# Kernel tuning notes

Measured on AMD Instinct MI355X. Metric: run time of the kernel, lower is better.

## Reference

```python
import jax, jax.numpy as jnp
import numpy as np

D, DFF, H = 768, 3072, 12
HD = D // H
EPS = 1e-12

def _ln(t, gamma, beta):
    mu = t.mean(-1, keepdims=True)
    var = jnp.mean((t - mu) ** 2, -1, keepdims=True)
    return gamma * (t - mu) / jnp.sqrt(var + EPS) + beta

def setup_inputs() -> dict:
    key = jax.random.key(0)
    ks = jax.random.split(key, 16)
    s = 0.02
    x = jax.random.normal(ks[0], (2, 2048, D), jnp.float32)
    mask = jnp.ones((2, 2048), jnp.float32)
    def lin(k, out_d, in_d):
        kw, kb = jax.random.split(k)
        return (jax.random.normal(kw, (out_d, in_d), jnp.float32) * s,
                jnp.zeros((out_d,), jnp.float32))
    Wq, bq = lin(ks[1], D, D)
    Wk, bk = lin(ks[2], D, D)
    Wv, bv = lin(ks[3], D, D)
    Wp, bp = lin(ks[4], D, D)
    W1, bf1 = lin(ks[5], DFF, D)
    W2, bf2 = lin(ks[6], D, DFF)
    g1 = jnp.ones((D,), jnp.float32); be1 = jnp.zeros((D,), jnp.float32)
    g2 = jnp.ones((D,), jnp.float32); be2 = jnp.zeros((D,), jnp.float32)
    return dict(x=x, mask=mask, Wq=Wq, bq=bq, Wk=Wk, bk=bk, Wv=Wv, bv=bv,
                Wp=Wp, bp=bp, g1=g1, be1=be1, W1=W1, bf1=bf1, W2=W2, bf2=bf2,
                g2=g2, be2=be2)

def reference(x, mask, Wq, bq, Wk, bk, Wv, bv, Wp, bp, g1, be1, W1, bf1, W2, bf2, g2, be2):
    B, S, _ = x.shape
    # projections (torch Linear: x @ W^T + b)
    q = (x @ Wq.T + bq).reshape(B, S, H, HD).transpose(0, 2, 1, 3)  # [B,H,S,HD]
    k = (x @ Wk.T + bk).reshape(B, S, H, HD).transpose(0, 2, 1, 3)
    v = (x @ Wv.T + bv).reshape(B, S, H, HD).transpose(0, 2, 1, 3)
    scores = jnp.einsum('bhqd,bhkd->bhqk', q, k) / jnp.sqrt(jnp.float32(HD))
    scores = scores - 10000.0 * (1.0 - mask[:, None, None, :])
    p = jax.nn.softmax(scores, axis=-1)  # dropout is identity at eval
    h = jnp.einsum('bhqk,bhkd->bqhd', p, v).reshape(B, S, D)
    h = h @ Wp.T + bp
    x1 = _ln(x + h, g1, be1)
    ff = jax.nn.gelu(x1 @ W1.T + bf1, approximate=False) @ W2.T + bf2
    return _ln(x1 + ff, g2, be2)
```

## Files before the change

### kernel.cpp

```cpp
#include <hip/hip_runtime.h>
#include <hip/hip_bf16.h>
#include <math.h>

#define D_MODEL 768
#define D_FF    3072
#define N_HEAD  12
#define HEAD_D  64
#define BATCH   2
#define SEQ     2048
#define QKV_LD  2304

typedef __attribute__((ext_vector_type(8))) short short8;
typedef __attribute__((ext_vector_type(8))) unsigned short ushort8;
typedef __attribute__((ext_vector_type(4))) float f32x4;

__device__ inline unsigned short f2bf(float f) {
    union { __hip_bfloat16 b; unsigned short u; } cv;
    cv.b = __float2bfloat16(f);
    return cv.u;
}

__device__ inline float bf2f(unsigned short u) {
    union { unsigned int i; float f; } cv;
    cv.i = ((unsigned int)u) << 16;
    return cv.f;
}

__device__ inline void async_load16(const void* g, void* l) {
    __builtin_amdgcn_global_load_lds(
        (const __attribute__((address_space(1))) void*)g,
        (__attribute__((address_space(3))) void*)l, 16, 0, 0);
}

__global__ __launch_bounds__(256) void conv_fused(
    const float* __restrict__ x,
    const float* __restrict__ Wq, const float* __restrict__ Wk,
    const float* __restrict__ Wv, const float* __restrict__ Wp,
    const float* __restrict__ W1, const float* __restrict__ W2,
    const float* __restrict__ bq, const float* __restrict__ bk,
    const float* __restrict__ bv,
    unsigned short* __restrict__ xb, unsigned short* __restrict__ wqkvb,
    unsigned short* __restrict__ wpb, unsigned short* __restrict__ w1b,
    unsigned short* __restrict__ w2b, float* __restrict__ bqkv)
{
    int bid = blockIdx.x;
    const float* src; unsigned short* dst; int base;
    if      (bid < 3072) { src = x;  dst = xb;              base = bid;        }
    else if (bid < 3648) { src = Wq; dst = wqkvb;           base = bid - 3072; }
    else if (bid < 4224) { src = Wk; dst = wqkvb + 589824;  base = bid - 3648; }
    else if (bid < 4800) { src = Wv; dst = wqkvb + 1179648; base = bid - 4224; }
    else if (bid < 5376) { src = Wp; dst = wpb;             base = bid - 4800; }
    else if (bid < 7680) { src = W1; dst = w1b;             base = bid - 5376; }
    else if (bid < 9984) { src = W2; dst = w2b;             base = bid - 7680; }
    else {
        for (int j = threadIdx.x; j < QKV_LD; j += 256)
            bqkv[j] = (j < 768) ? bq[j] : (j < 1536) ? bk[j - 768] : bv[j - 1536];
        return;
    }
    int i = (base * 256 + threadIdx.x) * 4;
    float4 v = *(const float4*)(src + i);
    ushort4 o4;
    o4.x = f2bf(v.x); o4.y = f2bf(v.y); o4.z = f2bf(v.z); o4.w = f2bf(v.w);
    *(ushort4*)(dst + i) = o4;
}

#define NSTAGE 3

__global__ __launch_bounds__(256) void gemm_bf16(
    const unsigned short* __restrict__ A, int lda,
    const unsigned short* __restrict__ W, int ldw,
    const float* __restrict__ bias,
    const unsigned short* __restrict__ resb, int ldr,
    float* __restrict__ outf, unsigned short* __restrict__ outb,
    float* __restrict__ pacc, int ldo,
    int M, int N, int K, int mode)
{
    __shared__ unsigned short As[NSTAGE][128 * 32];
    __shared__ unsigned short Bs[NSTAGE][128 * 32];

    const int t    = threadIdx.x;
    const int lane = t & 63;
    const int wv   = t >> 6;
    const int wm   = wv >> 1;
    const int wn   = wv & 1;
    const int bm   = blockIdx.y * 128;
    const int bn   = blockIdx.x * 128;
    const int kz   = blockIdx.z;
    const int Kc   = K / gridDim.z;

    const int qd   = lane >> 4;
    const int l16  = lane & 15;

    f32x4 acc[4][4];
    #pragma unroll
    for (int i = 0; i < 4; i++)
        #pragma unroll
        for (int j = 0; j < 4; j++)
            acc[i][j] = (f32x4){0.f, 0.f, 0.f, 0.f};

    const int srow = lane >> 2;
    const int sseg = (lane & 3) * 8;
    const int r0   = (wv * 2 + 0) * 16 + srow;
    const int r1   = (wv * 2 + 1) * 16 + srow;
    const size_t gA0 = (size_t)(bm + r0) * lda + sseg;
    const size_t gA1 = (size_t)(bm + r1) * lda + sseg;
    const size_t gB0 = (size_t)(bn + r0) * ldw + sseg;
    const size_t gB1 = (size_t)(bn + r1) * ldw + sseg;
    const int c0 = (wv * 2 + 0) * 512;
    const int c1 = (wv * 2 + 1) * 512;

    const int kbeg  = kz * Kc;
    const int niter = Kc / 32;

    async_load16(A + gA0 + kbeg, &As[0][c0]);
    async_load16(W + gB0 + kbeg, &Bs[0][c0]);
    async_load16(A + gA1 + kbeg, &As[0][c1]);
    async_load16(W + gB1 + kbeg, &Bs[0][c1]);
    if (niter > 1) {
        async_load16(A + gA0 + kbeg + 32, &As[1][c0]);
        async_load16(W + gB0 + kbeg + 32, &Bs[1][c0]);
        async_load16(A + gA1 + kbeg + 32, &As[1][c1]);
        async_load16(W + gB1 + kbeg + 32, &Bs[1][c1]);
    }

    int stage = 0;
    for (int it = 0; it < niter; it++) {
        if (it + 1 < niter) __builtin_amdgcn_s_waitcnt(0x0F74);
        else                __builtin_amdgcn_s_waitcnt(0x0F70);
        __builtin_amdgcn_s_barrier();

        if (it + 2 < niter) {
            const int sn = (stage + 2 >= NSTAGE) ? stage + 2 - NSTAGE : stage + 2;
            const int kn = kbeg + (it + 2) * 32;
            async_load16(A + gA0 + kn, &As[sn][c0]);
            async_load16(W + gB0 + kn, &Bs[sn][c0]);
            async_load16(A + gA1 + kn, &As[sn][c1]);
            async_load16(W + gB1 + kn, &Bs[sn][c1]);
        }

        short8 af[4], bf[4];
        #pragma unroll
        for (int mt = 0; mt < 4; mt++)
            af[mt] = *(const short8*)(&As[stage][(wm * 64 + mt * 16 + l16) * 32 + qd * 8]);
        #pragma unroll
        for (int nt = 0; nt < 4; nt++)
            bf[nt] = *(const short8*)(&Bs[stage][(wn * 64 + nt * 16 + l16) * 32 + qd * 8]);
        #pragma unroll
        for (int mt = 0; mt < 4; mt++)
            #pragma unroll
            for (int nt = 0; nt < 4; nt++)
                acc[mt][nt] = __builtin_amdgcn_mfma_f32_16x16x32_bf16(
                    af[mt], bf[nt], acc[mt][nt], 0, 0, 0);

        stage = (stage == NSTAGE - 1) ? 0 : stage + 1;
    }

    #pragma unroll
    for (int mt = 0; mt < 4; mt++) {
        #pragma unroll
        for (int nt = 0; nt < 4; nt++) {
            int col = bn + wn * 64 + nt * 16 + l16;
            float bv = (kz == 0) ? bias[col] : 0.f;
            #pragma unroll
            for (int r = 0; r < 4; r++) {
                int row = bm + wm * 64 + mt * 16 + qd * 4 + r;
                if (kz != 0) {
                    pacc[(size_t)row * ldo + col] = acc[mt][nt][r];
                    continue;
                }
                float v = acc[mt][nt][r] + bv;
                if (mode == 1) {
                    v += bf2f(resb[(size_t)row * ldr + col]);
                    outf[(size_t)row * ldo + col] = v;
                } else if (mode == 2) {
                    v = 0.5f * v * (1.0f + erff(v * 0.70710678118654752f));
                    outb[(size_t)row * ldo + col] = f2bf(v);
                } else if (mode == 3) {
                    outb[(size_t)row * ldo + col] = f2bf(v);
                } else {
                    outf[(size_t)row * ldo + col] = v;
                }
            }
        }
    }
}

__global__ __launch_bounds__(256) void gemm_qkv(
    const unsigned short* __restrict__ A,
    const unsigned short* __restrict__ W,
    const float* __restrict__ bias,
    unsigned short* __restrict__ outb)
{
    __shared__ unsigned short As[4][128 * 32];
    __shared__ unsigned short Bs[4][128 * 32];

    const int t    = threadIdx.x;
    const int lane = t & 63;
    const int wv   = t >> 6;
    const int wm   = wv >> 1;
    const int wn   = wv & 1;

    const int flat = blockIdx.y * 18 + blockIdx.x;
    const int xcd  = flat & 7;
    const int u    = flat >> 3;
    const int mi   = (xcd >> 1) * 8 + u / 9;
    const int ni   = (xcd & 1) * 9 + u % 9;
    const int bm   = mi * 128;
    const int bn   = ni * 128;

    const int qd   = lane >> 4;
    const int l16  = lane & 15;

    f32x4 acc[4][4];
    #pragma unroll
    for (int i = 0; i < 4; i++)
        #pragma unroll
        for (int j = 0; j < 4; j++)
            acc[i][j] = (f32x4){0.f, 0.f, 0.f, 0.f};

    const int srow = lane >> 2;
    const int sseg = (lane & 3) * 8;
    const int r0   = (wv * 2 + 0) * 16 + srow;
    const int r1   = (wv * 2 + 1) * 16 + srow;
    const size_t gA0 = (size_t)(bm + r0) * D_MODEL + sseg;
    const size_t gA1 = (size_t)(bm + r1) * D_MODEL + sseg;
    const size_t gB0 = (size_t)(bn + r0) * D_MODEL + sseg;
    const size_t gB1 = (size_t)(bn + r1) * D_MODEL + sseg;
    const int c0 = (wv * 2 + 0) * 512;
    const int c1 = (wv * 2 + 1) * 512;

    const int niter = D_MODEL / 32;

    async_load16(A + gA0, &As[0][c0]);
    async_load16(W + gB0, &Bs[0][c0]);
    async_load16(A + gA1, &As[0][c1]);
    async_load16(W + gB1, &Bs[0][c1]);
    async_load16(A + gA0 + 32, &As[1][c0]);
    async_load16(W + gB0 + 32, &Bs[1][c0]);
    async_load16(A + gA1 + 32, &As[1][c1]);
    async_load16(W + gB1 + 32, &Bs[1][c1]);
    async_load16(A + gA0 + 64, &As[2][c0]);
    async_load16(W + gB0 + 64, &Bs[2][c0]);
    async_load16(A + gA1 + 64, &As[2][c1]);
    async_load16(W + gB1 + 64, &Bs[2][c1]);

    int stage = 0;
    for (int it = 0; it < niter; it++) {
        if      (it + 2 < niter) __builtin_amdgcn_s_waitcnt(0x0F78);
        else if (it + 1 < niter) __builtin_amdgcn_s_waitcnt(0x0F74);
        else                     __builtin_amdgcn_s_waitcnt(0x0F70);
        __builtin_amdgcn_s_barrier();

        if (it + 3 < niter) {
            int sn = stage + 3;
            if (sn >= 4) sn -= 4;
            const int kn = (it + 3) * 32;
            async_load16(A + gA0 + kn, &As[sn][c0]);
            async_load16(W + gB0 + kn, &Bs[sn][c0]);
            async_load16(A + gA1 + kn, &As[sn][c1]);
            async_load16(W + gB1 + kn, &Bs[sn][c1]);
        }

        short8 af[4], bf[4];
        #pragma unroll
        for (int mt = 0; mt < 4; mt++)
            af[mt] = *(const short8*)(&As[stage][(wm * 64 + mt * 16 + l16) * 32 + qd * 8]);
        #pragma unroll
        for (int nt = 0; nt < 4; nt++)
            bf[nt] = *(const short8*)(&Bs[stage][(wn * 64 + nt * 16 + l16) * 32 + qd * 8]);
        #pragma unroll
        for (int mt = 0; mt < 4; mt++)
            #pragma unroll
            for (int nt = 0; nt < 4; nt++)
                acc[mt][nt] = __builtin_amdgcn_mfma_f32_16x16x32_bf16(
                    af[mt], bf[nt], acc[mt][nt], 0, 0, 0);

        stage = (stage == 3) ? 0 : stage + 1;
    }

    #pragma unroll
    for (int mt = 0; mt < 4; mt++) {
        #pragma unroll
        for (int nt = 0; nt < 4; nt++) {
            int col = bn + wn * 64 + nt * 16 + l16;
            float bv = bias[col];
            #pragma unroll
            for (int r = 0; r < 4; r++) {
                int row = bm + wm * 64 + mt * 16 + qd * 4 + r;
                outb[(size_t)row * QKV_LD + col] = f2bf(acc[mt][nt][r] + bv);
            }
        }
    }
}

__global__ __launch_bounds__(256) void gemm_ffn1(
    const unsigned short* __restrict__ A,
    const unsigned short* __restrict__ W,
    const float* __restrict__ bias,
    unsigned short* __restrict__ outb)
{
    __shared__ unsigned short As[NSTAGE][128 * 32];
    __shared__ unsigned short Bs[NSTAGE][128 * 32];

    const int t    = threadIdx.x;
    const int lane = t & 63;
    const int wv   = t >> 6;
    const int wm   = wv >> 1;
    const int wn   = wv & 1;

    const int flat = blockIdx.y * 24 + blockIdx.x;
    const int xcd  = flat & 7;
    const int u    = flat >> 3;
    const int mi   = (xcd >> 1) * 8 + u / 12;
    const int ni   = (xcd & 1) * 12 + u % 12;
    const int bm   = mi * 128;
    const int bn   = ni * 128;

    const int qd   = lane >> 4;
    const int l16  = lane & 15;

    f32x4 acc[4][4];
    #pragma unroll
    for (int i = 0; i < 4; i++)
        #pragma unroll
        for (int j = 0; j < 4; j++)
            acc[i][j] = (f32x4){0.f, 0.f, 0.f, 0.f};

    const int srow = lane >> 2;
    const int sseg = (lane & 3) * 8;
    const int r0   = (wv * 2 + 0) * 16 + srow;
    const int r1   = (wv * 2 + 1) * 16 + srow;
    const size_t gA0 = (size_t)(bm + r0) * D_MODEL + sseg;
    const size_t gA1 = (size_t)(bm + r1) * D_MODEL + sseg;
    const size_t gB0 = (size_t)(bn + r0) * D_MODEL + sseg;
    const size_t gB1 = (size_t)(bn + r1) * D_MODEL + sseg;
    const int c0 = (wv * 2 + 0) * 512;
    const int c1 = (wv * 2 + 1) * 512;

    const int niter = D_MODEL / 32;

    async_load16(A + gA0, &As[0][c0]);
    async_load16(W + gB0, &Bs[0][c0]);
    async_load16(A + gA1, &As[0][c1]);
    async_load16(W + gB1, &Bs[0][c1]);
    async_load16(A + gA0 + 32, &As[1][c0]);
    async_load16(W + gB0 + 32, &Bs[1][c0]);
    async_load16(A + gA1 + 32, &As[1][c1]);
    async_load16(W + gB1 + 32, &Bs[1][c1]);

    int stage = 0;
    for (int it = 0; it < niter; it++) {
        if (it + 1 < niter) __builtin_amdgcn_s_waitcnt(0x0F74);
        else                __builtin_amdgcn_s_waitcnt(0x0F70);
        __builtin_amdgcn_s_barrier();

        if (it + 2 < niter) {
            const int sn = (stage + 2 >= NSTAGE) ? stage + 2 - NSTAGE : stage + 2;
            const int kn = (it + 2) * 32;
            async_load16(A + gA0 + kn, &As[sn][c0]);
            async_load16(W + gB0 + kn, &Bs[sn][c0]);
            async_load16(A + gA1 + kn, &As[sn][c1]);
            async_load16(W + gB1 + kn, &Bs[sn][c1]);
        }

        short8 af[4], bf[4];
        #pragma unroll
        for (int mt = 0; mt < 4; mt++)
            af[mt] = *(const short8*)(&As[stage][(wm * 64 + mt * 16 + l16) * 32 + qd * 8]);
        #pragma unroll
        for (int nt = 0; nt < 4; nt++)
            bf[nt] = *(const short8*)(&Bs[stage][(wn * 64 + nt * 16 + l16) * 32 + qd * 8]);
        #pragma unroll
        for (int mt = 0; mt < 4; mt++)
            #pragma unroll
            for (int nt = 0; nt < 4; nt++)
                acc[mt][nt] = __builtin_amdgcn_mfma_f32_16x16x32_bf16(
                    af[mt], bf[nt], acc[mt][nt], 0, 0, 0);

        stage = (stage == NSTAGE - 1) ? 0 : stage + 1;
    }

    #pragma unroll
    for (int mt = 0; mt < 4; mt++) {
        #pragma unroll
        for (int nt = 0; nt < 4; nt++) {
            int col = bn + wn * 64 + nt * 16 + l16;
            float bv = bias[col];
            #pragma unroll
            for (int r = 0; r < 4; r++) {
                int row = bm + wm * 64 + mt * 16 + qd * 4 + r;
                float v = acc[mt][nt][r] + bv;
                v = 0.5f * v * (1.0f + erff(v * 0.70710678118654752f));
                outb[(size_t)row * D_FF + col] = f2bf(v);
            }
        }
    }
}

__global__ __launch_bounds__(256) void gemm_ffn2(
    const unsigned short* __restrict__ A,
    const unsigned short* __restrict__ W,
    const float* __restrict__ bias,
    const unsigned short* __restrict__ resb,
    float* __restrict__ outf,
    float* __restrict__ pacc)
{
    __shared__ unsigned short As[2][128 * 64];
    __shared__ unsigned short Bs[2][128 * 64];

    const int t    = threadIdx.x;
    const int lane = t & 63;
    const int wv   = t >> 6;
    const int wm   = wv >> 1;
    const int wn   = wv & 1;

    const int flat = blockIdx.x;
    const int g    = flat & 7;
    const int u    = flat >> 3;
    const int kz   = g >> 2;
    const int g2   = g & 3;
    const int band = u / 24;
    const int rr   = (u % 24) / 6;
    const int cc   = u % 6;
    const int bm   = (g2 * 8 + band * 4 + rr) * 128;
    const int bn   = cc * 128;

    const int qd   = lane >> 4;
    const int l16  = lane & 15;

    f32x4 acc[4][4];
    #pragma unroll
    for (int i = 0; i < 4; i++)
        #pragma unroll
        for (int j = 0; j < 4; j++)
            acc[i][j] = (f32x4){0.f, 0.f, 0.f, 0.f};

    const int srow8 = lane >> 3;
    const int scol  = ((lane & 7) ^ srow8) * 8;
    const size_t gA_base = (size_t)(bm + wv * 32 + srow8) * D_FF + scol;
    const size_t gB_base = (size_t)(bn + wv * 32 + srow8) * D_FF + scol;
    const int ldsb = wv * 4 * 512;

    const int kbeg  = kz * (D_FF / 2);
    const int niter = (D_FF / 2) / 64;

    #pragma unroll
    for (int j = 0; j < 4; j++) {
        async_load16(A + gA_base + (size_t)(j * 8) * D_FF + kbeg, &As[0][ldsb + j * 512]);
        async_load16(W + gB_base + (size_t)(j * 8) * D_FF + kbeg, &Bs[0][ldsb + j * 512]);
    }

    for (int it = 0; it < niter; it++) {
        __builtin_amdgcn_s_waitcnt(0x0F70);
        __builtin_amdgcn_s_barrier();
        const int st = it & 1;

        if (it + 1 < niter) {
            const int kn = kbeg + (it + 1) * 64;
            #pragma unroll
            for (int j = 0; j < 4; j++) {
                async_load16(A + gA_base + (size_t)(j * 8) * D_FF + kn, &As[st ^ 1][ldsb + j * 512]);
                async_load16(W + gB_base + (size_t)(j * 8) * D_FF + kn, &Bs[st ^ 1][ldsb + j * 512]);
            }
        }

        #pragma unroll
        for (int kk = 0; kk < 2; kk++) {
            short8 af[4], bf[4];
            #pragma unroll
            for (int mt = 0; mt < 4; mt++) {
                const int row = wm * 64 + mt * 16 + l16;
                const int slot = (kk * 4 + qd) ^ (row & 7);
                af[mt] = *(const short8*)&As[st][row * 64 + slot * 8];
            }
            #pragma unroll
            for (int nt = 0; nt < 4; nt++) {
                const int row = wn * 64 + nt * 16 + l16;
                const int slot = (kk * 4 + qd) ^ (row & 7);
                bf[nt] = *(const short8*)&Bs[st][row * 64 + slot * 8];
            }
            #pragma unroll
            for (int mt = 0; mt < 4; mt++)
                #pragma unroll
                for (int nt = 0; nt < 4; nt++)
                    acc[mt][nt] = __builtin_amdgcn_mfma_f32_16x16x32_bf16(
                        af[mt], bf[nt], acc[mt][nt], 0, 0, 0);
        }
    }

    #pragma unroll
    for (int mt = 0; mt < 4; mt++) {
        #pragma unroll
        for (int nt = 0; nt < 4; nt++) {
            int col = bn + wn * 64 + nt * 16 + l16;
            #pragma unroll
            for (int r = 0; r < 4; r++) {
                int row = bm + wm * 64 + mt * 16 + qd * 4 + r;
                if (kz != 0) {
                    pacc[(size_t)row * D_MODEL + col] = acc[mt][nt][r];
                } else {
                    float v = acc[mt][nt][r] + bias[col]
                            + bf2f(resb[(size_t)row * D_MODEL + col]);
                    outf[(size_t)row * D_MODEL + col] = v;
                }
            }
        }
    }
}

__global__ __launch_bounds__(256) void vtrans(
    const unsigned short* __restrict__ qkv, unsigned short* __restrict__ vT)
{
    __shared__ unsigned short T[64 * 72];
    const int t   = threadIdx.x;
    const int kt  = blockIdx.x;
    const int bh  = blockIdx.y;
    const int h   = bh % N_HEAD;
    const int b   = bh / N_HEAD;
    const int row = t >> 2;
    const int c0  = (t & 3) * 16;

    const unsigned short* src =
        qkv + (size_t)(b * SEQ + kt * 64 + row) * QKV_LD + 1536 + h * HEAD_D + c0;
    *(ushort8*)&T[row * 72 + c0]     = *(const ushort8*)src;
    *(ushort8*)&T[row * 72 + c0 + 8] = *(const ushort8*)(src + 8);
    __syncthreads();

    const int d = t >> 2;
    ushort8 o0, o1;
    #pragma unroll
    for (int j = 0; j < 8; j++) o0[j] = T[(c0 + j) * 72 + d];
    #pragma unroll
    for (int j = 0; j < 8; j++) o1[j] = T[(c0 + 8 + j) * 72 + d];
    unsigned short* dst = vT + ((size_t)bh * HEAD_D + d) * SEQ + kt * 64 + c0;
    *(ushort8*)dst       = o0;
    *(ushort8*)(dst + 8) = o1;
}

#define ASTR 72
#define VSTR 136

__global__ __launch_bounds__(256) void attn_mfma(
    const unsigned short* __restrict__ qkv, const unsigned short* __restrict__ vT,
    const float* __restrict__ mask, unsigned short* __restrict__ out)
{
    __shared__ __align__(16) unsigned short Ks[128 * ASTR];
    __shared__ __align__(16) unsigned short Vt[64 * VSTR];
    __shared__ float Ms[128];

    const int t    = threadIdx.x;
    const int lane = t & 63;
    const int wv   = t >> 6;
    const int l16  = lane & 15;
    const int quad = lane >> 4;
    const int q0   = blockIdx.x * 64;
    const int bh   = blockIdx.y;
    const int h    = bh % N_HEAD;
    const int b    = bh / N_HEAD;
    const int NT   = SEQ / 128;

    const unsigned short* qb  = qkv + (size_t)b * SEQ * QKV_LD + h * HEAD_D;
    const unsigned short* kb  = qb + 768;
    const unsigned short* vtb = vT + (size_t)bh * HEAD_D * SEQ;

    {
        const int qsrow = t >> 2;
        const int qsc0  = (t & 3) * 16;
        const ushort8* src = (const ushort8*)(qb + (size_t)(q0 + qsrow) * QKV_LD + qsc0);
        *(ushort8*)&Ks[qsrow * ASTR + qsc0]     = src[0];
        *(ushort8*)&Ks[qsrow * ASTR + qsc0 + 8] = src[1];
    }
    __syncthreads();
    short8 bq0 = *(const short8*)&Ks[(wv * 16 + l16) * ASTR + quad * 8];
    short8 bq1 = *(const short8*)&Ks[(wv * 16 + l16) * ASTR + 32 + quad * 8];
    __syncthreads();

    const int krow_s = t >> 1;
    const int kc0    = (t & 1) * 32;
    const int ks6    = krow_s & 63;
    const int ksig   = (krow_s & 64) |
                       ((ks6 & 0x23) | ((ks6 & 0x04) << 2) | ((ks6 & 0x18) >> 1));
    const int vrow_s = t >> 2;
    const int vc0    = (t & 3) * 32;

    f32x4 o[4];
    #pragma unroll
    for (int i = 0; i < 4; i++) o[i] = (f32x4){0.f, 0.f, 0.f, 0.f};
    float m_st = -INFINITY, l_st = 0.f;

    ushort8 rk0, rk1, rk2, rk3, rv0, rv1, rv2, rv3;
    float rm = 1.0f;
    {
        const ushort8* ksrc = (const ushort8*)(kb + (size_t)krow_s * QKV_LD + kc0);
        rk0 = ksrc[0]; rk1 = ksrc[1]; rk2 = ksrc[2]; rk3 = ksrc[3];
        const ushort8* vsrc = (const ushort8*)(vtb + (size_t)vrow_s * SEQ + vc0);
        rv0 = vsrc[0]; rv1 = vsrc[1]; rv2 = vsrc[2]; rv3 = vsrc[3];
        if (t < 128) rm = mask[b * SEQ + t];
    }

    for (int kt = 0; kt < NT; kt++) {
        *(ushort8*)&Ks[ksig * ASTR + kc0]      = rk0;
        *(ushort8*)&Ks[ksig * ASTR + kc0 + 8]  = rk1;
        *(ushort8*)&Ks[ksig * ASTR + kc0 + 16] = rk2;
        *(ushort8*)&Ks[ksig * ASTR + kc0 + 24] = rk3;
        *(ushort8*)&Vt[vrow_s * VSTR + vc0]      = rv0;
        *(ushort8*)&Vt[vrow_s * VSTR + vc0 + 8]  = rv1;
        *(ushort8*)&Vt[vrow_s * VSTR + vc0 + 16] = rv2;
        *(ushort8*)&Vt[vrow_s * VSTR + vc0 + 24] = rv3;
        if (t < 128) Ms[t] = -10000.0f * (1.0f - rm);
        __syncthreads();

        if (kt + 1 < NT) {
            const int kn = (kt + 1) * 128;
            const ushort8* ksrc = (const ushort8*)(kb + (size_t)(kn + krow_s) * QKV_LD + kc0);
            rk0 = ksrc[0]; rk1 = ksrc[1]; rk2 = ksrc[2]; rk3 = ksrc[3];
            const ushort8* vsrc = (const ushort8*)(vtb + (size_t)vrow_s * SEQ + kn + vc0);
            rv0 = vsrc[0]; rv1 = vsrc[1]; rv2 = vsrc[2]; rv3 = vsrc[3];
            if (t < 128) rm = mask[b * SEQ + kn + t];
        }

        float p[8][4];
        float mx = -3.0e38f;
        #pragma unroll
        for (int bi = 0; bi < 8; bi++) {
            const int krow = (bi * 16 + l16) * ASTR;
            short8 k0 = *(const short8*)&Ks[krow + quad * 8];
            short8 k1 = *(const short8*)&Ks[krow + 32 + quad * 8];
            f32x4 z = (f32x4){0.f, 0.f, 0.f, 0.f};
            z = __builtin_amdgcn_mfma_f32_16x16x32_bf16(k0, bq0, z, 0, 0, 0);
            z = __builtin_amdgcn_mfma_f32_16x16x32_bf16(k1, bq1, z, 0, 0, 0);
            const float4 m4 = *(const float4*)
                &Ms[(bi >> 2) * 64 + ((bi >> 1) & 1) * 32 + quad * 8 + (bi & 1) * 4];
            #pragma unroll
            for (int r = 0; r < 4; r++) {
                float s = fmaf(z[r], 0.125f, ((const float*)&m4)[r]);
                p[bi][r] = s;
                mx = fmaxf(mx, s);
            }
        }
        mx = fmaxf(mx, __shfl_xor(mx, 16, 64));
        mx = fmaxf(mx, __shfl_xor(mx, 32, 64));
        float m_new = fmaxf(m_st, mx);
        float alpha = __expf(m_st - m_new);
        m_st = m_new;
        float ls = 0.f;
        #pragma unroll
        for (int bi = 0; bi < 8; bi++) {
            #pragma unroll
            for (int r = 0; r < 4; r++) {
                p[bi][r] = __expf(p[bi][r] - m_new);
                ls += p[bi][r];
            }
        }
        ls += __shfl_xor(ls, 16, 64);
        ls += __shfl_xor(ls, 32, 64);
        l_st = l_st * alpha + ls;

        float ar[4];
        #pragma unroll
        for (int r = 0; r < 4; r++) ar[r] = __shfl(alpha, quad * 4 + r, 64);
        #pragma unroll
        for (int nt = 0; nt < 4; nt++)
            #pragma unroll
            for (int r = 0; r < 4; r++)
                o[nt][r] *= ar[r];

        short8 pf[4];
        #pragma unroll
        for (int w = 0; w < 4; w++) {
            #pragma unroll
            for (int bsel = 0; bsel < 2; bsel++) {
                #pragma unroll
                for (int r = 0; r < 4; r++)
                    pf[w][bsel * 4 + r] = (short)f2bf(p[w * 2 + bsel][r]);
            }
        }

        #pragma unroll
        for (int nt = 0; nt < 4; nt++) {
            const int vrow = (nt * 16 + l16) * VSTR;
            #pragma unroll
            for (int w = 0; w < 4; w++) {
                short8 vv = *(const short8*)&Vt[vrow + w * 32 + quad * 8];
                o[nt] = __builtin_amdgcn_mfma_f32_16x16x32_bf16(pf[w], vv, o[nt], 0, 0, 0);
            }
        }
        __syncthreads();
    }

    float inv = 1.0f / l_st;
    float ir[4];
    #pragma unroll
    for (int r = 0; r < 4; r++) ir[r] = __shfl(inv, quad * 4 + r, 64);
    #pragma unroll
    for (int nt = 0; nt < 4; nt++) {
        #pragma unroll
        for (int r = 0; r < 4; r++) {
            int qi = q0 + wv * 16 + quad * 4 + r;
            out[(size_t)(b * SEQ + qi) * D_MODEL + h * HEAD_D + nt * 16 + l16] =
                f2bf(o[nt][r] * ir[r]);
        }
    }
}

__global__ __launch_bounds__(256) void ln_kernel(
    const float* __restrict__ in, const float* __restrict__ in2,
    const float* __restrict__ g, const float* __restrict__ be,
    float* __restrict__ outf, unsigned short* __restrict__ outb)
{
    const int row = blockIdx.x;
    const int t   = threadIdx.x;
    const float* rp  = in  + (size_t)row * D_MODEL;
    const float* rp2 = in2 ? in2 + (size_t)row * D_MODEL : nullptr;

    float vals[3];
    float s = 0.f, s2 = 0.f;
    #pragma unroll
    for (int i = 0; i < 3; i++) {
        float x = rp[t + i * 256];
        if (rp2) x += rp2[t + i * 256];
        vals[i] = x;
        s += x; s2 += x * x;
    }
    #pragma unroll
    for (int off = 32; off >= 1; off >>= 1) {
        s  += __shfl_xor(s,  off, 64);
        s2 += __shfl_xor(s2, off, 64);
    }
    __shared__ float rs[4], rs2[4];
    __shared__ float mu_s, rstd_s;
    const int wave = t >> 6, lane = t & 63;
    if (lane == 0) { rs[wave] = s; rs2[wave] = s2; }
    __syncthreads();
    if (t == 0) {
        float S1 = rs[0] + rs[1] + rs[2] + rs[3];
        float S2 = rs2[0] + rs2[1] + rs2[2] + rs2[3];
        float mu  = S1 * (1.0f / D_MODEL);
        float var = S2 * (1.0f / D_MODEL) - mu * mu;
        mu_s = mu;
        rstd_s = rsqrtf(var + 1e-12f);
    }
    __syncthreads();
    const float mu = mu_s, rstd = rstd_s;
    #pragma unroll
    for (int i = 0; i < 3; i++) {
        int c = t + i * 256;
        float o = g[c] * (vals[i] - mu) * rstd + be[c];
        if (outf) outf[(size_t)row * D_MODEL + c] = o;
        if (outb) outb[(size_t)row * D_MODEL + c] = f2bf(o);
    }
}

extern "C" void kernel_launch(void* const* d_in, const int* in_sizes, int n_in,
                              void* d_out, int out_size, void* d_ws, size_t ws_size,
                              hipStream_t stream)
{
    const float* x    = (const float*)d_in[0];
    const float* mask = (const float*)d_in[1];
    const float* Wq   = (const float*)d_in[2];
    const float* bq   = (const float*)d_in[3];
    const float* Wk   = (const float*)d_in[4];
    const float* bk   = (const float*)d_in[5];
    const float* Wv   = (const float*)d_in[6];
    const float* bv   = (const float*)d_in[7];
    const float* Wp   = (const float*)d_in[8];
    const float* bp   = (const float*)d_in[9];
    const float* g1   = (const float*)d_in[10];
    const float* be1  = (const float*)d_in[11];
    const float* W1   = (const float*)d_in[12];
    const float* bf1  = (const float*)d_in[13];
    const float* W2   = (const float*)d_in[14];
    const float* bf2  = (const float*)d_in[15];
    const float* g2   = (const float*)d_in[16];
    const float* be2  = (const float*)d_in[17];

    const int M = BATCH * SEQ;

    char* ws = (char*)d_ws;
    unsigned short* qkvb  = (unsigned short*)(ws + 0);
    unsigned short* ff1b  = (unsigned short*)(ws + 0);
    unsigned short* xb    = (unsigned short*)(ws + 25165824);
    unsigned short* hb    = (unsigned short*)(ws + 31457280);
    unsigned short* x1b   = (unsigned short*)(ws + 31457280);
    float*          y0    = (float*)(ws + 37748736);
    unsigned short* wqkvb = (unsigned short*)(ws + 50331648);
    unsigned short* wpb   = (unsigned short*)(ws + 53870592);
    unsigned short* w1b   = (unsigned short*)(ws + 55050240);
    unsigned short* w2b   = (unsigned short*)(ws + 59768832);
    float*          bqkv  = (float*)(ws + 64487424);
    float*          p1    = (float*)(ws + 64496640);
    unsigned short* vTb   = (unsigned short*)(ws + 77079552);

    dim3 blk(256);

    conv_fused<<<dim3(9985), blk, 0, stream>>>(
        x, Wq, Wk, Wv, Wp, W1, W2, bq, bk, bv,
        xb, wqkvb, wpb, w1b, w2b, bqkv);

    gemm_qkv<<<dim3(QKV_LD / 128, M / 128), blk, 0, stream>>>(xb, wqkvb, bqkv, qkvb);

    vtrans<<<dim3(SEQ / 64, BATCH * N_HEAD), blk, 0, stream>>>(qkvb, vTb);

    attn_mfma<<<dim3(SEQ / 64, BATCH * N_HEAD), blk, 0, stream>>>(qkvb, vTb, mask, hb);

    gemm_bf16<<<dim3(D_MODEL / 128, M / 128, 2), blk, 0, stream>>>(
        hb, D_MODEL, wpb, D_MODEL, bp, xb, D_MODEL,
        y0, nullptr, p1, D_MODEL, M, D_MODEL, D_MODEL, 1);

    ln_kernel<<<dim3(M), blk, 0, stream>>>(y0, p1, g1, be1, nullptr, x1b);

    gemm_ffn1<<<dim3(D_FF / 128, M / 128), blk, 0, stream>>>(x1b, w1b, bf1, ff1b);

    gemm_ffn2<<<dim3(384), blk, 0, stream>>>(ff1b, w2b, bf2, x1b, y0, p1);

    ln_kernel<<<dim3(M), blk, 0, stream>>>(y0, p1, g2, be2, (float*)d_out, nullptr);
}
```

Measured before the change: 336.0 us.

## Use BK=64 double-buffered tiles with XOR-swizzled LDS in QKV and FFN1 GEMMs

New measurement: 352.5 us. +4.9%, slower.

```diff
diff --git a/kernel.cpp b/kernel.cpp
--- a/kernel.cpp
+++ b/kernel.cpp
@@ -191,8 +191,8 @@
     const float* __restrict__ bias,
     unsigned short* __restrict__ outb)
 {
-    __shared__ unsigned short As[4][128 * 32];
-    __shared__ unsigned short Bs[4][128 * 32];
+    __shared__ unsigned short As[2][128 * 64];
+    __shared__ unsigned short Bs[2][128 * 64];
 
     const int t    = threadIdx.x;
     const int lane = t & 63;
@@ -218,64 +218,56 @@
         for (int j = 0; j < 4; j++)
             acc[i][j] = (f32x4){0.f, 0.f, 0.f, 0.f};
 
-    const int srow = lane >> 2;
-    const int sseg = (lane & 3) * 8;
-    const int r0   = (wv * 2 + 0) * 16 + srow;
-    const int r1   = (wv * 2 + 1) * 16 + srow;
-    const size_t gA0 = (size_t)(bm + r0) * D_MODEL + sseg;
-    const size_t gA1 = (size_t)(bm + r1) * D_MODEL + sseg;
-    const size_t gB0 = (size_t)(bn + r0) * D_MODEL + sseg;
-    const size_t gB1 = (size_t)(bn + r1) * D_MODEL + sseg;
-    const int c0 = (wv * 2 + 0) * 512;
-    const int c1 = (wv * 2 + 1) * 512;
-
-    const int niter = D_MODEL / 32;
-
-    async_load16(A + gA0, &As[0][c0]);
-    async_load16(W + gB0, &Bs[0][c0]);
-    async_load16(A + gA1, &As[0][c1]);
-    async_load16(W + gB1, &Bs[0][c1]);
-    async_load16(A + gA0 + 32, &As[1][c0]);
-    async_load16(W + gB0 + 32, &Bs[1][c0]);
-    async_load16(A + gA1 + 32, &As[1][c1]);
-    async_load16(W + gB1 + 32, &Bs[1][c1]);
-    async_load16(A + gA0 + 64, &As[2][c0]);
-    async_load16(W + gB0 + 64, &Bs[2][c0]);
-    async_load16(A + gA1 + 64, &As[2][c1]);
-    async_load16(W + gB1 + 64, &Bs[2][c1]);
-
-    int stage = 0;
+    const int srow8 = lane >> 3;
+    const int scol  = ((lane & 7) ^ srow8) * 8;
+    const size_t gA_base = (size_t)(bm + wv * 32 + srow8) * D_MODEL + scol;
+    const size_t gB_base = (size_t)(bn + wv * 32 + srow8) * D_MODEL + scol;
+    const int ldsb = wv * 4 * 512;
+
+    const int niter = D_MODEL / 64;
+
+    #pragma unroll
+    for (int j = 0; j < 4; j++) {
+        async_load16(A + gA_base + (size_t)(j * 8) * D_MODEL, &As[0][ldsb + j * 512]);
+        async_load16(W + gB_base + (size_t)(j * 8) * D_MODEL, &Bs[0][ldsb + j * 512]);
+    }
+
     for (int it = 0; it < niter; it++) {
-        if      (it + 2 < niter) __builtin_amdgcn_s_waitcnt(0x0F78);
-        else if (it + 1 < niter) __builtin_amdgcn_s_waitcnt(0x0F74);
-        else                     __builtin_amdgcn_s_waitcnt(0x0F70);
+        __builtin_amdgcn_s_waitcnt(0x0F70);
         __builtin_amdgcn_s_barrier();
-
-        if (it + 3 < niter) {
-            int sn = stage + 3;
-            if (sn >= 4) sn -= 4;
-            const int kn = (it + 3) * 32;
-            async_load16(A + gA0 + kn, &As[sn][c0]);
-            async_load16(W + gB0 + kn, &Bs[sn][c0]);
-            async_load16(A + gA1 + kn, &As[sn][c1]);
-            async_load16(W + gB1 + kn, &Bs[sn][c1]);
-        }
-
-        short8 af[4], bf[4];
-        #pragma unroll
-        for (int mt = 0; mt < 4; mt++)
-            af[mt] = *(const short8*)(&As[stage][(wm * 64 + mt * 16 + l16) * 32 + qd * 8]);
-        #pragma unroll
-        for (int nt = 0; nt < 4; nt++)
-            bf[nt] = *(const short8*)(&Bs[stage][(wn * 64 + nt * 16 + l16) * 32 + qd * 8]);
-        #pragma unroll
-        for (int mt = 0; mt < 4; mt++)
-            #pragma unroll
-            for (int nt = 0; nt < 4; nt++)
-                acc[mt][nt] = __builtin_amdgcn_mfma_f32_16x16x32_bf16(
-                    af[mt], bf[nt], acc[mt][nt], 0, 0, 0);
-
-        stage = (stage == 3) ? 0 : stage + 1;
+        const int st = it & 1;
+
+        if (it + 1 < niter) {
+            const int kn = (it + 1) * 64;
+            #pragma unroll
+            for (int j = 0; j < 4; j++) {
+                async_load16(A + gA_base + (size_t)(j * 8) * D_MODEL + kn, &As[st ^ 1][ldsb + j * 512]);
+                async_load16(W + gB_base + (size_t)(j * 8) * D_MODEL + kn, &Bs[st ^ 1][ldsb + j * 512]);
+            }
+        }
+
+        #pragma unroll
+        for (int kk = 0; kk < 2; kk++) {
+            short8 af[4], bf[4];
+            #pragma unroll
+            for (int mt = 0; mt < 4; mt++) {
+                const int row = wm * 64 + mt * 16 + l16;
+                const int slot = (kk * 4 + qd) ^ (row & 7);
+                af[mt] = *(const short8*)&As[st][row * 64 + slot * 8];
+            }
+            #pragma unroll
+            for (int nt = 0; nt < 4; nt++) {
+                const int row = wn * 64 + nt * 16 + l16;
+                const int slot = (kk * 4 + qd) ^ (row & 7);
+                bf[nt] = *(const short8*)&Bs[st][row * 64 + slot * 8];
+            }
+            #pragma unroll
+            for (int mt = 0; mt < 4; mt++)
+                #pragma unroll
+                for (int nt = 0; nt < 4; nt++)
+                    acc[mt][nt] = __builtin_amdgcn_mfma_f32_16x16x32_bf16(
+                        af[mt], bf[nt], acc[mt][nt], 0, 0, 0);
+        }
     }
 
     #pragma unroll
@@ -299,8 +291,8 @@
     const float* __restrict__ bias,
     unsigned short* __restrict__ outb)
 {
-    __shared__ unsigned short As[NSTAGE][128 * 32];
-    __shared__ unsigned short Bs[NSTAGE][128 * 32];
+    __shared__ unsigned short As[2][128 * 64];
+    __shared__ unsigned short Bs[2][128 * 64];
 
     const int t    = threadIdx.x;
     const int lane = t & 63;
@@ -326,58 +318,56 @@
         for (int j = 0; j < 4; j++)
             acc[i][j] = (f32x4){0.f, 0.f, 0.f, 0.f};
 
-    const int srow = lane >> 2;
-    const int sseg = (lane & 3) * 8;
-    const int r0   = (wv * 2 + 0) * 16 + srow;
-    const int r1   = (wv * 2 + 1) * 16 + srow;
-    const size_t gA0 = (size_t)(bm + r0) * D_MODEL + sseg;
-    const size_t gA1 = (size_t)(bm + r1) * D_MODEL + sseg;
-    const size_t gB0 = (size_t)(bn + r0) * D_MODEL + sseg;
-    const size_t gB1 = (size_t)(bn + r1) * D_MODEL + sseg;
-    const int c0 = (wv * 2 + 0) * 512;
-    const int c1 = (wv * 2 + 1) * 512;
-
-    const int niter = D_MODEL / 32;
-
-    async_load16(A + gA0, &As[0][c0]);
-    async_load16(W + gB0, &Bs[0][c0]);
-    async_load16(A + gA1, &As[0][c1]);
-    async_load16(W + gB1, &Bs[0][c1]);
-    async_load16(A + gA0 + 32, &As[1][c0]);
-    async_load16(W + gB0 + 32, &Bs[1][c0]);
-    async_load16(A + gA1 + 32, &As[1][c1]);
-    async_load16(W + gB1 + 32, &Bs[1][c1]);
-
-    int stage = 0;
+    const int srow8 = lane >> 3;
+    const int scol  = ((lane & 7) ^ srow8) * 8;
+    const size_t gA_base = (size_t)(bm + wv * 32 + srow8) * D_MODEL + scol;
+    const size_t gB_base = (size_t)(bn + wv * 32 + srow8) * D_MODEL + scol;
+    const int ldsb = wv * 4 * 512;
+
+    const int niter = D_MODEL / 64;
+
+    #pragma unroll
+    for (int j = 0; j < 4; j++) {
+        async_load16(A + gA_base + (size_t)(j * 8) * D_MODEL, &As[0][ldsb + j * 512]);
+        async_load16(W + gB_base + (size_t)(j * 8) * D_MODEL, &Bs[0][ldsb + j * 512]);
+    }
+
     for (int it = 0; it < niter; it++) {
-        if (it + 1 < niter) __builtin_amdgcn_s_waitcnt(0x0F74);
-        else                __builtin_amdgcn_s_waitcnt(0x0F70);
+        __builtin_amdgcn_s_waitcnt(0x0F70);
         __builtin_amdgcn_s_barrier();
-
-        if (it + 2 < niter) {
-            const int sn = (stage + 2 >= NSTAGE) ? stage + 2 - NSTAGE : stage + 2;
-            const int kn = (it + 2) * 32;
-            async_load16(A + gA0 + kn, &As[sn][c0]);
-            async_load16(W + gB0 + kn, &Bs[sn][c0]);
-            async_load16(A + gA1 + kn, &As[sn][c1]);
-            async_load16(W + gB1 + kn, &Bs[sn][c1]);
-        }
-
-        short8 af[4], bf[4];
-        #pragma unroll
-        for (int mt = 0; mt < 4; mt++)
-            af[mt] = *(const short8*)(&As[stage][(wm * 64 + mt * 16 + l16) * 32 + qd * 8]);
-        #pragma unroll
-        for (int nt = 0; nt < 4; nt++)
-            bf[nt] = *(const short8*)(&Bs[stage][(wn * 64 + nt * 16 + l16) * 32 + qd * 8]);
-        #pragma unroll
-        for (int mt = 0; mt < 4; mt++)
-            #pragma unroll
-            for (int nt = 0; nt < 4; nt++)
-                acc[mt][nt] = __builtin_amdgcn_mfma_f32_16x16x32_bf16(
-                    af[mt], bf[nt], acc[mt][nt], 0, 0, 0);
-
-        stage = (stage == NSTAGE - 1) ? 0 : stage + 1;
+        const int st = it & 1;
+
+        if (it + 1 < niter) {
+            const int kn = (it + 1) * 64;
+            #pragma unroll
+            for (int j = 0; j < 4; j++) {
+                async_load16(A + gA_base + (size_t)(j * 8) * D_MODEL + kn, &As[st ^ 1][ldsb + j * 512]);
+                async_load16(W + gB_base + (size_t)(j * 8) * D_MODEL + kn, &Bs[st ^ 1][ldsb + j * 512]);
+            }
+        }
+
+        #pragma unroll
+        for (int kk = 0; kk < 2; kk++) {
+            short8 af[4], bf[4];
+            #pragma unroll
+            for (int mt = 0; mt < 4; mt++) {
+                const int row = wm * 64 + mt * 16 + l16;
+                const int slot = (kk * 4 + qd) ^ (row & 7);
+                af[mt] = *(const short8*)&As[st][row * 64 + slot * 8];
+            }
+            #pragma unroll
+            for (int nt = 0; nt < 4; nt++) {
+                const int row = wn * 64 + nt * 16 + l16;
+                const int slot = (kk * 4 + qd) ^ (row & 7);
+                bf[nt] = *(const short8*)&Bs[st][row * 64 + slot * 8];
+            }
+            #pragma unroll
+            for (int mt = 0; mt < 4; mt++)
+                #pragma unroll
+                for (int nt = 0; nt < 4; nt++)
+                    acc[mt][nt] = __builtin_amdgcn_mfma_f32_16x16x32_bf16(
+                        af[mt], bf[nt], acc[mt][nt], 0, 0, 0);
+        }
     }
 
     #pragma unroll
```
